# Kernel tuning notes

Measured on AMD Instinct MI355X. Metric: run time of the kernel, lower is better.

Reference implementation:

```python
import jax, jax.numpy as jnp
import numpy as np
from jax import lax

VOCAB, EMB, H, L, B = 32000, 512, 512, 256, 64


def _flip_bwd(t):
    # t: (L, B, 2, ...); reverse time for the backward direction (dir index 1)
    return jnp.stack([t[:, :, 0], t[::-1, :, 1]], axis=2)


def sru_layer(x, W, bias, k, n_out):
    """Bidirectional SRU layer.
    x: (L, B, n_in); W: (n_in, 2*n_out*k); bias: (2, 2, n_out) = (gate{f,r}, dir, n_out).
    k=4: 4th projection is the highway input; k=3: highway uses x itself (n_in == 2*n_out).
    """
    Lx, Bx, _ = x.shape
    u = (x @ W).reshape(Lx, Bx, 2, n_out, k)
    u = _flip_bwd(u)  # both directions now scan forward in time
    f = jax.nn.sigmoid(u[..., 1] + bias[0][None, None])  # (L,B,2,n_out)
    r = jax.nn.sigmoid(u[..., 2] + bias[1][None, None])
    x_tilde = u[..., 0]

    def step(c, inp):
        f_t, xt = inp
        c = f_t * c + (1.0 - f_t) * xt
        return c, c

    c0 = jnp.zeros((Bx, 2, n_out), x.dtype)
    c_last, cs = lax.scan(step, c0, (f, x_tilde))

    if k == 4:
        x_res = u[..., 3]
    else:
        x_res = _flip_bwd(x.reshape(Lx, Bx, 2, n_out))
    h = r * jnp.tanh(cs) + (1.0 - r) * x_res
    h = _flip_bwd(h)  # restore true time order for backward dir
    return h.reshape(Lx, Bx, 2 * n_out), c_last.reshape(Bx, 2 * n_out)


def setup_inputs() -> dict:
    key = jax.random.key(0)
    ks = jax.random.split(key, 8)
    inp = {
        'padded_encoder_inputs': jax.random.randint(ks[0], (L, B), 0, VOCAB),
        'emb': jax.random.normal(ks[1], (VOCAB, EMB), jnp.float32) * 0.1,
        'W0': jax.random.normal(ks[2], (EMB, 2 * H * 4), jnp.float32) * 0.05,
        'b0': jax.random.normal(ks[3], (2, 2, H), jnp.float32) * 0.05,
        'W1': jax.random.normal(ks[4], (2 * H, 2 * H * 3), jnp.float32) * 0.05,
        'b1': jax.random.normal(ks[5], (2, 2, H), jnp.float32) * 0.05,
        'Wd': jax.random.normal(ks[6], (H, 2 * H), jnp.float32) * 0.05,
        'bd': jax.random.normal(ks[7], (H,), jnp.float32) * 0.05,
    }
    return inp


def reference(padded_encoder_inputs, emb, W0, b0, W1, b1, Wd, bd):
    # embedding lookup (dropout layers are identity in eval mode)
    x = emb[padded_encoder_inputs]            # (L, B, EMB)
    h1, c1 = sru_layer(x, W0, b0, 4, H)       # (L,B,2H), (B,2H)
    h2, c2 = sru_layer(h1, W1, b1, 3, H)
    hidden = jnp.stack([c1, c2], axis=0)      # (layers, B, 2H)
    hidden = hidden @ Wd.T + bd               # dense_hidden: (layers, B, H)
    return h2, hidden
```

## Files before the change

kernel.cpp:

```cpp
#include <hip/hip_runtime.h>

typedef __attribute__((ext_vector_type(8))) short bf16x8;
typedef __attribute__((ext_vector_type(4))) float f32x4;

__device__ __forceinline__ float b2f(ushort s) { return __uint_as_float(((uint)s) << 16); }
__device__ __forceinline__ ushort f2b(float f) {
  uint u = __float_as_uint(f);
  u += 0x7fff + ((u >> 16) & 1);
  return (ushort)(u >> 16);
}

__device__ __forceinline__ void store_h(float* p, float v) { *p = v; }
__device__ __forceinline__ void store_h(ushort* p, float v) { *p = f2b(v); }

__device__ __forceinline__ float sigm_fast(float x) { return 1.f / (1.f + __expf(-x)); }
__device__ __forceinline__ float tanh_fast(float c) {
  float e = __expf(-2.f * fabsf(c));
  float t = (1.f - e) / (1.f + e);
  return copysignf(t, c);
}

__global__ void transpose_kernel(const float* __restrict__ in, ushort* __restrict__ out,
                                 int R, int C) {
  __shared__ ushort tile[32][33];
  int bc = blockIdx.x << 5;
  int br = blockIdx.y << 5;
  int tx = threadIdx.x & 31;
  int ty = threadIdx.x >> 5;
#pragma unroll
  for (int i = 0; i < 32; i += 8)
    tile[ty + i][tx] = f2b(in[(size_t)(br + ty + i) * C + bc + tx]);
  __syncthreads();
#pragma unroll
  for (int i = 0; i < 32; i += 8)
    out[(size_t)(bc + ty + i) * R + br + tx] = tile[tx][ty + i];
}

__global__ void embed_kernel(const int* __restrict__ tok, const float* __restrict__ emb,
                             ushort* __restrict__ x) {
  int tid = threadIdx.x;
  int r = (blockIdx.x << 2) + (tid >> 6);
  int c = (tid & 63) << 3;
  int t = tok[r];
  const float* src = emb + ((size_t)t << 9) + c;
  float4 a = *(const float4*)src;
  float4 b = *(const float4*)(src + 4);
  uint4 o;
  o.x = (uint)f2b(a.x) | ((uint)f2b(a.y) << 16);
  o.y = (uint)f2b(a.z) | ((uint)f2b(a.w) << 16);
  o.z = (uint)f2b(b.x) | ((uint)f2b(b.y) << 16);
  o.w = (uint)f2b(b.z) | ((uint)f2b(b.w) << 16);
  *(uint4*)(x + ((size_t)r << 9) + c) = o;
}

__global__ __launch_bounds__(512, 1) void gemm_bt5_kernel(
    const ushort* __restrict__ A, const ushort* __restrict__ BT,
    ushort* __restrict__ C, int M, int N, int K) {
  __shared__ char lds[2][65536];
  const int tid = threadIdx.x;
  const int lane = tid & 63;
  const int wave = tid >> 6;
  const int wr = wave >> 2;
  const int wc = wave & 3;

  const int xcd = blockIdx.x & 7;
  const int l = blockIdx.x >> 3;
  const int s = xcd * (gridDim.x >> 8) + (l >> 5);
  const int uu = l & 31;
  const int mt = ((s & 7) << 3) + (uu & 7);
  const int nt = ((s >> 3) << 2) + (uu >> 3);
  const int m0 = mt << 8;
  const int n0 = nt << 8;
  const int NT = K >> 6;

  const int k0s = ((lane >> 4) << 4) ^ ((lane & 7) << 4);
  const int aB0 = (wr << 14) + ((lane & 15) << 7) + k0s;
  const int aB1 = aB0 ^ 64;
  const int bB0 = 32768 + (wc << 13) + ((lane & 15) << 7) + k0s;
  const int bB1 = bB0 ^ 64;

  int srcoff[4];
#pragma unroll
  for (int sub = 0; sub < 4; ++sub) {
    int off = (sub << 13) + (tid << 4);
    int row = off >> 7;
    int col = ((off & 127) ^ ((row & 7) << 4)) >> 1;
    srcoff[sub] = row * K + col;
  }
  const ushort* Abase = A + (size_t)m0 * K;
  const ushort* Bbase = BT + (size_t)n0 * K;

  auto stage = [&](int t, int p) {
    const int tk = t << 6;
#pragma unroll
    for (int i = 0; i < 8; ++i) {
      int sub = i & 3;
      const ushort* src = ((i < 4) ? Abase : Bbase) + srcoff[sub] + tk;
      char* dst = lds[p] + ((i < 4) ? 0 : 32768) + (sub << 13) + (wave << 10);
      __builtin_amdgcn_global_load_lds(
          (const __attribute__((address_space(1))) void*)src,
          (__attribute__((address_space(3))) void*)dst, 16, 0, 0);
    }
  };

  f32x4 acc[8][4];
#pragma unroll
  for (int i = 0; i < 8; ++i)
#pragma unroll
    for (int j = 0; j < 4; ++j) acc[i][j] = (f32x4){0.f, 0.f, 0.f, 0.f};

  stage(0, 0);
  for (int t = 0; t < NT; ++t) {
    int p = t & 1;
    if (t + 1 < NT) {
      stage(t + 1, p ^ 1);
      asm volatile("s_waitcnt vmcnt(8)" ::: "memory");
    } else {
      asm volatile("s_waitcnt vmcnt(0)" ::: "memory");
    }
    __builtin_amdgcn_s_barrier();
    const char* base = (const char*)lds[0] + (p << 16);
    bf16x8 afA[8], bgA[4], afB[8], bgB[4];
#pragma unroll
    for (int mi = 0; mi < 8; ++mi) afA[mi] = *(const bf16x8*)(base + aB0 + (mi << 11));
#pragma unroll
    for (int ni = 0; ni < 4; ++ni) bgA[ni] = *(const bf16x8*)(base + bB0 + (ni << 11));
#pragma unroll
    for (int mi = 0; mi < 8; ++mi) afB[mi] = *(const bf16x8*)(base + aB1 + (mi << 11));
#pragma unroll
    for (int ni = 0; ni < 4; ++ni) bgB[ni] = *(const bf16x8*)(base + bB1 + (ni << 11));
    __builtin_amdgcn_s_setprio(1);
#pragma unroll
    for (int mi = 0; mi < 8; ++mi)
#pragma unroll
      for (int ni = 0; ni < 4; ++ni)
        acc[mi][ni] =
            __builtin_amdgcn_mfma_f32_16x16x32_bf16(afA[mi], bgA[ni], acc[mi][ni], 0, 0, 0);
#pragma unroll
    for (int mi = 0; mi < 8; ++mi)
#pragma unroll
      for (int ni = 0; ni < 4; ++ni)
        acc[mi][ni] =
            __builtin_amdgcn_mfma_f32_16x16x32_bf16(afB[mi], bgB[ni], acc[mi][ni], 0, 0, 0);
    __builtin_amdgcn_s_setprio(0);
    __builtin_amdgcn_s_barrier();
  }
#pragma unroll
  for (int mi = 0; mi < 8; ++mi) {
#pragma unroll
    for (int j = 0; j < 4; ++j) {
      int row = m0 + (wr << 7) + (mi << 4) + ((lane >> 4) << 2) + j;
      size_t bofs = (size_t)row * N + n0 + (wc << 6);
#pragma unroll
      for (int ni = 0; ni < 4; ++ni)
        C[bofs + (ni << 4) + (lane & 15)] = f2b(acc[mi][ni][j]);
    }
  }
}

template <int KC, typename OT>
__global__ void sru_scan_kernel(const ushort* __restrict__ u, const float* __restrict__ bias,
                                const ushort* __restrict__ xres, OT* __restrict__ hout,
                                float* __restrict__ cout) {
  const int L = 256, B = 64, H = 512;
  int idx = blockIdx.x * 256 + threadIdx.x;
  int h = idx & (H - 1);
  int dir = (idx >> 9) & 1;
  int b = idx >> 10;
  float bfg = bias[dir * H + h];
  float brg = bias[2 * H + dir * H + h];
  const size_t ustep = (size_t)B * 2 * H * KC;
  const ushort* ubase = u + ((size_t)b * 2 + dir) * H * KC + (size_t)h * KC;
  const size_t hstep = (size_t)B * 2 * H;
  const size_t hoff = (size_t)b * 2 * H + (size_t)dir * H + h;
  float c = 0.f;
#pragma unroll 16
  for (int s = 0; s < L; ++s) {
    int t = dir ? (L - 1 - s) : s;
    const ushort* up = ubase + (size_t)t * ustep;
    float xt, fg, rg, xr;
    if (KC == 4) {
      uint2 v = *(const uint2*)up;
      xt = b2f((ushort)(v.x & 0xffff));
      fg = b2f((ushort)(v.x >> 16));
      rg = b2f((ushort)(v.y & 0xffff));
      xr = b2f((ushort)(v.y >> 16));
    } else {
      xt = b2f(up[0]);
      fg = b2f(up[1]);
      rg = b2f(up[2]);
      xr = b2f(xres[hoff + (size_t)t * hstep]);
    }
    float f = sigm_fast(fg + bfg);
    float r = sigm_fast(rg + brg);
    c = f * c + (1.f - f) * xt;
    float hv = r * tanh_fast(c) + (1.f - r) * xr;
    store_h(hout + hoff + (size_t)t * hstep, hv);
  }
  cout[(size_t)b * 2 * H + (size_t)dir * H + h] = c;
}

__global__ __launch_bounds__(512) void dense_kernel(
    const float* __restrict__ c12, const ushort* __restrict__ WdT,
    const float* __restrict__ bd, float* __restrict__ out) {
  int row = blockIdx.x;
  int j = threadIdx.x;
  const float* c = c12 + (size_t)row * 1024;
  float acc = bd[j];
#pragma unroll 8
  for (int k = 0; k < 1024; ++k) acc += c[k] * b2f(WdT[(size_t)k * 512 + j]);
  out[(size_t)row * 512 + j] = acc;
}

extern "C" void kernel_launch(void* const* d_in, const int* in_sizes, int n_in,
                              void* d_out, int out_size, void* d_ws, size_t ws_size,
                              hipStream_t stream) {
  const int* tok = (const int*)d_in[0];
  const float* emb = (const float*)d_in[1];
  const float* W0 = (const float*)d_in[2];
  const float* b0 = (const float*)d_in[3];
  const float* W1 = (const float*)d_in[4];
  const float* b1 = (const float*)d_in[5];
  const float* Wd = (const float*)d_in[6];
  const float* bd = (const float*)d_in[7];
  float* out = (float*)d_out;

  char* ws = (char*)d_ws;
  ushort* x = (ushort*)ws;
  ushort* W0T = (ushort*)(ws + 16777216);
  ushort* W1T = (ushort*)(ws + 20971520);
  ushort* u = (ushort*)(ws + 27262976);
  ushort* h1 = (ushort*)(ws + 161480704);
  float* c12 = (float*)(ws + 195035136);
  ushort* WdT = (ushort*)(ws + 27262976 + 100663296);

  transpose_kernel<<<dim3(128, 16), 256, 0, stream>>>(W0, W0T, 512, 4096);
  transpose_kernel<<<dim3(96, 32), 256, 0, stream>>>(W1, W1T, 1024, 3072);
  embed_kernel<<<4096, 256, 0, stream>>>(tok, emb, x);
  gemm_bt5_kernel<<<1024, 512, 0, stream>>>(x, W0T, u, 16384, 4096, 512);
  sru_scan_kernel<4, ushort><<<256, 256, 0, stream>>>(u, b0, (const ushort*)nullptr, h1, c12);
  gemm_bt5_kernel<<<768, 512, 0, stream>>>(h1, W1T, u, 16384, 3072, 1024);
  sru_scan_kernel<3, float><<<256, 256, 0, stream>>>(u, b1, h1, out, c12 + 65536);
  transpose_kernel<<<dim3(32, 16), 256, 0, stream>>>(Wd, WdT, 512, 1024);
  dense_kernel<<<128, 512, 0, stream>>>(c12, WdT, bd, out + 16777216);
}
```

Measured before the change: 366.0 us.

## Split GEMM k-step into four MFMA phases interleaved with LDS reads and prefetch

```diff
diff --git a/kernel.cpp b/kernel.cpp
--- a/kernel.cpp
+++ b/kernel.cpp
@@ -53,7 +53,7 @@
   *(uint4*)(x + ((size_t)r << 9) + c) = o;
 }
 
-__global__ __launch_bounds__(512, 1) void gemm_bt5_kernel(
+__global__ __launch_bounds__(512, 1) void gemm_bt6_kernel(
     const ushort* __restrict__ A, const ushort* __restrict__ BT,
     ushort* __restrict__ C, int M, int N, int K) {
   __shared__ char lds[2][65536];
@@ -90,10 +90,10 @@
   const ushort* Abase = A + (size_t)m0 * K;
   const ushort* Bbase = BT + (size_t)n0 * K;
 
-  auto stage = [&](int t, int p) {
+  auto stage4 = [&](int t, int p, int i0) {
     const int tk = t << 6;
 #pragma unroll
-    for (int i = 0; i < 8; ++i) {
+    for (int i = i0; i < i0 + 4; ++i) {
       int sub = i & 3;
       const ushort* src = ((i < 4) ? Abase : Bbase) + srcoff[sub] + tk;
       char* dst = lds[p] + ((i < 4) ? 0 : 32768) + (sub << 13) + (wave << 10);
@@ -109,42 +109,81 @@
 #pragma unroll
     for (int j = 0; j < 4; ++j) acc[i][j] = (f32x4){0.f, 0.f, 0.f, 0.f};
 
-  stage(0, 0);
+  stage4(0, 0, 0);
+  stage4(0, 0, 4);
+  asm volatile("s_waitcnt vmcnt(0)" ::: "memory");
+  __builtin_amdgcn_s_barrier();
+
   for (int t = 0; t < NT; ++t) {
-    int p = t & 1;
-    if (t + 1 < NT) {
-      stage(t + 1, p ^ 1);
-      asm volatile("s_waitcnt vmcnt(8)" ::: "memory");
-    } else {
-      asm volatile("s_waitcnt vmcnt(0)" ::: "memory");
-    }
-    __builtin_amdgcn_s_barrier();
+    const int p = t & 1;
     const char* base = (const char*)lds[0] + (p << 16);
-    bf16x8 afA[8], bgA[4], afB[8], bgB[4];
-#pragma unroll
-    for (int mi = 0; mi < 8; ++mi) afA[mi] = *(const bf16x8*)(base + aB0 + (mi << 11));
-#pragma unroll
-    for (int ni = 0; ni < 4; ++ni) bgA[ni] = *(const bf16x8*)(base + bB0 + (ni << 11));
-#pragma unroll
-    for (int mi = 0; mi < 8; ++mi) afB[mi] = *(const bf16x8*)(base + aB1 + (mi << 11));
-#pragma unroll
-    for (int ni = 0; ni < 4; ++ni) bgB[ni] = *(const bf16x8*)(base + bB1 + (ni << 11));
-    __builtin_amdgcn_s_setprio(1);
-#pragma unroll
-    for (int mi = 0; mi < 8; ++mi)
-#pragma unroll
-      for (int ni = 0; ni < 4; ++ni)
-        acc[mi][ni] =
-            __builtin_amdgcn_mfma_f32_16x16x32_bf16(afA[mi], bgA[ni], acc[mi][ni], 0, 0, 0);
-#pragma unroll
-    for (int mi = 0; mi < 8; ++mi)
-#pragma unroll
-      for (int ni = 0; ni < 4; ++ni)
-        acc[mi][ni] =
-            __builtin_amdgcn_mfma_f32_16x16x32_bf16(afB[mi], bgB[ni], acc[mi][ni], 0, 0, 0);
-    __builtin_amdgcn_s_setprio(0);
-    __builtin_amdgcn_s_barrier();
-  }
+    const bool pre = (t + 1 < NT);
+    bf16x8 af[4], bg0[4], bg1[4];
+
+#pragma unroll
+    for (int mi = 0; mi < 4; ++mi) af[mi] = *(const bf16x8*)(base + aB0 + (mi << 11));
+#pragma unroll
+    for (int ni = 0; ni < 4; ++ni) bg0[ni] = *(const bf16x8*)(base + bB0 + (ni << 11));
+    if (pre) stage4(t + 1, p ^ 1, 0);
+    __builtin_amdgcn_sched_barrier(0);
+    __builtin_amdgcn_s_barrier();
+    __builtin_amdgcn_s_setprio(1);
+#pragma unroll
+    for (int mi = 0; mi < 4; ++mi)
+#pragma unroll
+      for (int ni = 0; ni < 4; ++ni)
+        acc[mi][ni] = __builtin_amdgcn_mfma_f32_16x16x32_bf16(af[mi], bg0[ni], acc[mi][ni], 0, 0, 0);
+    __builtin_amdgcn_s_setprio(0);
+    __builtin_amdgcn_sched_barrier(0);
+    __builtin_amdgcn_s_barrier();
+
+#pragma unroll
+    for (int mi = 0; mi < 4; ++mi) af[mi] = *(const bf16x8*)(base + aB0 + ((mi + 4) << 11));
+    if (pre) stage4(t + 1, p ^ 1, 4);
+    __builtin_amdgcn_sched_barrier(0);
+    __builtin_amdgcn_s_barrier();
+    __builtin_amdgcn_s_setprio(1);
+#pragma unroll
+    for (int mi = 0; mi < 4; ++mi)
+#pragma unroll
+      for (int ni = 0; ni < 4; ++ni)
+        acc[mi + 4][ni] = __builtin_amdgcn_mfma_f32_16x16x32_bf16(af[mi], bg0[ni], acc[mi + 4][ni], 0, 0, 0);
+    __builtin_amdgcn_s_setprio(0);
+    __builtin_amdgcn_sched_barrier(0);
+    __builtin_amdgcn_s_barrier();
+
+#pragma unroll
+    for (int mi = 0; mi < 4; ++mi) af[mi] = *(const bf16x8*)(base + aB1 + (mi << 11));
+#pragma unroll
+    for (int ni = 0; ni < 4; ++ni) bg1[ni] = *(const bf16x8*)(base + bB1 + (ni << 11));
+    __builtin_amdgcn_sched_barrier(0);
+    __builtin_amdgcn_s_barrier();
+    __builtin_amdgcn_s_setprio(1);
+#pragma unroll
+    for (int mi = 0; mi < 4; ++mi)
+#pragma unroll
+      for (int ni = 0; ni < 4; ++ni)
+        acc[mi][ni] = __builtin_amdgcn_mfma_f32_16x16x32_bf16(af[mi], bg1[ni], acc[mi][ni], 0, 0, 0);
+    __builtin_amdgcn_s_setprio(0);
+    __builtin_amdgcn_sched_barrier(0);
+    __builtin_amdgcn_s_barrier();
+
+#pragma unroll
+    for (int mi = 0; mi < 4; ++mi) af[mi] = *(const bf16x8*)(base + aB1 + ((mi + 4) << 11));
+    __builtin_amdgcn_sched_barrier(0);
+    __builtin_amdgcn_s_barrier();
+    __builtin_amdgcn_s_setprio(1);
+#pragma unroll
+    for (int mi = 0; mi < 4; ++mi)
+#pragma unroll
+      for (int ni = 0; ni < 4; ++ni)
+        acc[mi + 4][ni] = __builtin_amdgcn_mfma_f32_16x16x32_bf16(af[mi], bg1[ni], acc[mi + 4][ni], 0, 0, 0);
+    __builtin_amdgcn_s_setprio(0);
+    __builtin_amdgcn_sched_barrier(0);
+    asm volatile("s_waitcnt vmcnt(0)" ::: "memory");
+    __builtin_amdgcn_s_barrier();
+  }
+
 #pragma unroll
   for (int mi = 0; mi < 8; ++mi) {
 #pragma unroll
@@ -237,9 +276,9 @@
   transpose_kernel<<<dim3(128, 16), 256, 0, stream>>>(W0, W0T, 512, 4096);
   transpose_kernel<<<dim3(96, 32), 256, 0, stream>>>(W1, W1T, 1024, 3072);
   embed_kernel<<<4096, 256, 0, stream>>>(tok, emb, x);
-  gemm_bt5_kernel<<<1024, 512, 0, stream>>>(x, W0T, u, 16384, 4096, 512);
+  gemm_bt6_kernel<<<1024, 512, 0, stream>>>(x, W0T, u, 16384, 4096, 512);
   sru_scan_kernel<4, ushort><<<256, 256, 0, stream>>>(u, b0, (const ushort*)nullptr, h1, c12);
-  gemm_bt5_kernel<<<768, 512, 0, stream>>>(h1, W1T, u, 16384, 3072, 1024);
+  gemm_bt6_kernel<<<768, 512, 0, stream>>>(h1, W1T, u, 16384, 3072, 1024);
   sru_scan_kernel<3, float><<<256, 256, 0, stream>>>(u, b1, h1, out, c12 + 65536);
   transpose_kernel<<<dim3(32, 16), 256, 0, stream>>>(Wd, WdT, 512, 1024);
   dense_kernel<<<128, 512, 0, stream>>>(c12, WdT, bd, out + 16777216);
```

New measurement: 365.6 us. No clear change (-0.1%).

## Parallelize SRU recurrence over time chunks with two-pass prefix combine

Applied to the files above, without the earlier changes.

```diff
diff --git a/kernel.cpp b/kernel.cpp
--- a/kernel.cpp
+++ b/kernel.cpp
@@ -159,24 +159,30 @@
 }
 
 template <int KC, typename OT>
-__global__ void sru_scan_kernel(const ushort* __restrict__ u, const float* __restrict__ bias,
-                                const ushort* __restrict__ xres, OT* __restrict__ hout,
-                                float* __restrict__ cout) {
-  const int L = 256, B = 64, H = 512;
-  int idx = blockIdx.x * 256 + threadIdx.x;
-  int h = idx & (H - 1);
-  int dir = (idx >> 9) & 1;
-  int b = idx >> 10;
-  float bfg = bias[dir * H + h];
-  float brg = bias[2 * H + dir * H + h];
-  const size_t ustep = (size_t)B * 2 * H * KC;
-  const ushort* ubase = u + ((size_t)b * 2 + dir) * H * KC + (size_t)h * KC;
-  const size_t hstep = (size_t)B * 2 * H;
-  const size_t hoff = (size_t)b * 2 * H + (size_t)dir * H + h;
-  float c = 0.f;
-#pragma unroll 16
-  for (int s = 0; s < L; ++s) {
-    int t = dir ? (L - 1 - s) : s;
+__global__ __launch_bounds__(256, 1) void sru_scan_chunked(
+    const ushort* __restrict__ u, const float* __restrict__ bias,
+    const ushort* __restrict__ xres, OT* __restrict__ hout, float* __restrict__ cout) {
+  const int L = 256, CL = 32;
+  __shared__ float Psh[256], Ssh[256];
+  const int tid = threadIdx.x;
+  const int j = tid >> 5;
+  const int chl = tid & 31;
+  const int ch = blockIdx.x * 32 + chl;
+  const int h = ch & 511;
+  const int dir = (ch >> 9) & 1;
+  const float bfg = bias[dir * 512 + h];
+  const float brg = bias[1024 + dir * 512 + h];
+  const size_t ustep = (size_t)65536 * KC;
+  const ushort* ubase = u + (size_t)ch * KC;
+  const size_t hstep = 65536;
+  const int t0 = dir ? (L - 1 - j * CL) : (j * CL);
+  const int tstep = dir ? -1 : 1;
+
+  float fv[CL], gv[CL], rv[CL], rx[CL];
+  float c = 0.f, P = 1.f;
+#pragma unroll
+  for (int s = 0; s < CL; ++s) {
+    int t = t0 + s * tstep;
     const ushort* up = ubase + (size_t)t * ustep;
     float xt, fg, rg, xr;
     if (KC == 4) {
@@ -189,15 +195,34 @@
       xt = b2f(up[0]);
       fg = b2f(up[1]);
       rg = b2f(up[2]);
-      xr = b2f(xres[hoff + (size_t)t * hstep]);
+      xr = b2f(xres[ch + (size_t)t * hstep]);
     }
     float f = sigm_fast(fg + bfg);
     float r = sigm_fast(rg + brg);
-    c = f * c + (1.f - f) * xt;
-    float hv = r * tanh_fast(c) + (1.f - r) * xr;
-    store_h(hout + hoff + (size_t)t * hstep, hv);
-  }
-  cout[(size_t)b * 2 * H + (size_t)dir * H + h] = c;
+    fv[s] = f;
+    gv[s] = (1.f - f) * xt;
+    rv[s] = r;
+    rx[s] = (1.f - r) * xr;
+    c = f * c + gv[s];
+    P *= f;
+  }
+  Psh[(chl << 3) + j] = P;
+  Ssh[(chl << 3) + j] = c;
+  __syncthreads();
+  float cin = 0.f;
+#pragma unroll
+  for (int k = 0; k < 7; ++k) {
+    if (k < j) cin = Psh[(chl << 3) + k] * cin + Ssh[(chl << 3) + k];
+  }
+  c = cin;
+#pragma unroll
+  for (int s = 0; s < CL; ++s) {
+    int t = t0 + s * tstep;
+    c = fv[s] * c + gv[s];
+    float hv = rv[s] * tanh_fast(c) + rx[s];
+    store_h(hout + ch + (size_t)t * hstep, hv);
+  }
+  if (j == 7) cout[ch] = c;
 }
 
 __global__ __launch_bounds__(512) void dense_kernel(
@@ -238,9 +263,9 @@
   transpose_kernel<<<dim3(96, 32), 256, 0, stream>>>(W1, W1T, 1024, 3072);
   embed_kernel<<<4096, 256, 0, stream>>>(tok, emb, x);
   gemm_bt5_kernel<<<1024, 512, 0, stream>>>(x, W0T, u, 16384, 4096, 512);
-  sru_scan_kernel<4, ushort><<<256, 256, 0, stream>>>(u, b0, (const ushort*)nullptr, h1, c12);
+  sru_scan_chunked<4, ushort><<<2048, 256, 0, stream>>>(u, b0, (const ushort*)nullptr, h1, c12);
   gemm_bt5_kernel<<<768, 512, 0, stream>>>(h1, W1T, u, 16384, 3072, 1024);
-  sru_scan_kernel<3, float><<<256, 256, 0, stream>>>(u, b1, h1, out, c12 + 65536);
+  sru_scan_chunked<3, float><<<2048, 256, 0, stream>>>(u, b1, h1, out, c12 + 65536);
   transpose_kernel<<<dim3(32, 16), 256, 0, stream>>>(Wd, WdT, 512, 1024);
   dense_kernel<<<128, 512, 0, stream>>>(c12, WdT, bd, out + 16777216);
 }
```

Result: no change. 364.2 us (-0.5%).
